# Performance work log

Hardware: AMD Instinct MI355X
Metric: run time of the kernel (lower is better)

The kernel has to match this reference:

```python
import jax, jax.numpy as jnp
import numpy as np

B = 8
S_MAX = 1024
H = 12
HD = 64
D = H * HD
DFF = 4 * D
NEG = -1.0e9  # matches Triton kernel's -1000000000.0 mask value


def _layernorm(x, g, b, eps=1e-6):
    mu = jnp.mean(x, axis=-1, keepdims=True)
    var = jnp.mean((x - mu) ** 2, axis=-1, keepdims=True)
    return (x - mu) * jax.lax.rsqrt(var + eps) * g + b


def setup_inputs() -> dict:
    key = jax.random.key(0)
    ks = jax.random.split(key, 12)
    lengths = np.array([1024, 896, 768, 640, 896, 1024, 512, 384], dtype=np.int32)
    assert lengths.max() <= S_MAX and len(lengths) == B
    total = int(lengths.sum())  # 6144
    cu = jnp.asarray(np.concatenate([[0], np.cumsum(lengths)]), dtype=jnp.int32)
    s = 0.02
    return {
        "x": jax.random.normal(ks[0], (total, D), jnp.float32),
        "cu_seqlens": cu,
        "g1": jnp.ones((D,), jnp.float32),
        "beta1": jnp.zeros((D,), jnp.float32),
        "Wqkv": jax.random.normal(ks[1], (D, 3 * D), jnp.float32) * s,
        "bqkv": jnp.zeros((3 * D,), jnp.float32),
        "Wo": jax.random.normal(ks[2], (D, D), jnp.float32) * s,
        "bo": jnp.zeros((D,), jnp.float32),
        "g2": jnp.ones((D,), jnp.float32),
        "beta2": jnp.zeros((D,), jnp.float32),
        "W1": jax.random.normal(ks[3], (D, DFF), jnp.float32) * s,
        "b_fc1": jnp.zeros((DFF,), jnp.float32),
        "W2": jax.random.normal(ks[4], (DFF, D), jnp.float32) * s,
        "b_fc2": jnp.zeros((D,), jnp.float32),
    }


def _ragged_attention(q, k, v, cu_seqlens):
    # q,k,v: [Total, H, HD] packed ragged sequences; cu_seqlens: [B+1] int32
    total = q.shape[0]
    lens = cu_seqlens[1:] - cu_seqlens[:-1]                      # [B]
    s = jnp.arange(S_MAX)
    pad_idx = cu_seqlens[:-1, None] + jnp.minimum(s[None, :], lens[:, None] - 1)  # [B,S]
    valid = s[None, :] < lens[:, None]                           # [B,S]
    qp = q[pad_idx]                                              # [B,S,H,HD]
    kp = k[pad_idx]
    vp = v[pad_idx]
    scale = 1.0 / jnp.sqrt(jnp.float32(HD))
    scores = jnp.einsum("bqhd,bkhd->bhqk", qp, kp) * scale      # [B,H,S,S]
    scores = jnp.where(valid[:, None, None, :], scores, NEG)     # mask invalid keys
    p = jax.nn.softmax(scores, axis=-1)
    op = jnp.einsum("bhqk,bkhd->bqhd", p, vp)                   # [B,S,H,HD]
    # repack to [Total, H, HD]
    tok = jnp.arange(total)
    seg = jnp.searchsorted(cu_seqlens, tok, side="right") - 1    # sequence id per token
    pos = tok - cu_seqlens[seg]
    return op[seg, pos]


def _forward(x, cu_seqlens, g1, beta1, Wqkv, bqkv, Wo, bo, g2, beta2, W1, b_fc1, W2, b_fc2):
    total = x.shape[0]
    qkv = (_layernorm(x, g1, beta1) @ Wqkv + bqkv).reshape(total, 3, H, HD)
    q, k, v = qkv[:, 0], qkv[:, 1], qkv[:, 2]
    attn = _ragged_attention(q, k, v, cu_seqlens).reshape(total, D)
    x = x + (attn @ Wo + bo)                                     # proj_drop/ls1/drop_path identity (eval)
    h = _layernorm(x, g2, beta2)
    m = jax.nn.gelu(h @ W1 + b_fc1, approximate=False)
    return x + (m @ W2 + b_fc2)


def reference(x, cu_seqlens, g1, beta1, Wqkv, bqkv, Wo, bo, g2, beta2, W1, b_fc1, W2, b_fc2):
    return _forward(x, cu_seqlens, g1, beta1, Wqkv, bqkv, Wo, bo, g2, beta2, W1, b_fc1, W2, b_fc2)
```

## Files before the change

kernel.cpp:

```cpp
#include <hip/hip_runtime.h>
#include <hip/hip_bf16.h>
#include <stdint.h>
#include <string.h>

#define D_MODEL 768
#define H_HEADS 12
#define HD_ 64
#define N_QKV 2304

typedef __bf16 bf16x8 __attribute__((ext_vector_type(8)));
typedef float f32x4 __attribute__((ext_vector_type(4)));

__device__ __forceinline__ unsigned short f2bfbits(float f) {
  union { float f; unsigned u; } x; x.f = f;
  unsigned r = x.u + 0x7fffu + ((x.u >> 16) & 1u);
  return (unsigned short)(r >> 16);
}

__device__ __forceinline__ unsigned pk2(float a, float b) {
  union { float f; unsigned u; } x, y; x.f = a; y.f = b;
  return ((x.u + 0x8000u) >> 16) | ((y.u + 0x8000u) & 0xffff0000u);
}

#define FENCE_() __builtin_amdgcn_sched_barrier(0)
__device__ __forceinline__ void store_sync() {
  FENCE_();
  asm volatile("s_waitcnt lgkmcnt(0)");
  FENCE_();
  __builtin_amdgcn_s_barrier();
  FENCE_();
}

__global__ void transpose_w(const float* __restrict__ in, unsigned short* __restrict__ out,
                            int R, int C) {
  __shared__ float tile[32][33];
  int c0 = blockIdx.x * 32, r0 = blockIdx.y * 32;
  int tx = threadIdx.x, ty = threadIdx.y;
#pragma unroll
  for (int i = 0; i < 32; i += 8)
    tile[ty + i][tx] = in[(size_t)(r0 + ty + i) * C + c0 + tx];
  __syncthreads();
#pragma unroll
  for (int i = 0; i < 32; i += 8)
    out[(size_t)(c0 + ty + i) * R + r0 + tx] = f2bfbits(tile[tx][ty + i]);
}

__global__ void transpose_v(const unsigned short* __restrict__ qkv,
                            unsigned short* __restrict__ vT, int M) {
  __shared__ unsigned short tile[32][33];
  int t0 = blockIdx.x * 32, c0 = blockIdx.y * 32;
  int tx = threadIdx.x, ty = threadIdx.y;
#pragma unroll
  for (int i = 0; i < 32; i += 8)
    tile[ty + i][tx] = qkv[(size_t)(t0 + ty + i) * N_QKV + 1536 + c0 + tx];
  __syncthreads();
  int t = t0 + tx;
  int c = t & 63;
  int kp = ((c >> 5) << 5) | (((c >> 2) & 3) << 3) | (((c >> 4) & 1) << 2) | (c & 3);
  size_t col = (size_t)(t & ~63) + kp;
#pragma unroll
  for (int i = 0; i < 32; i += 8)
    vT[(size_t)(c0 + ty + i) * M + col] = tile[tx][ty + i];
}

__global__ void ln_bf16(const float* __restrict__ x, const float* __restrict__ g,
                        const float* __restrict__ be, unsigned short* __restrict__ out) {
  int row = blockIdx.x;
  const float* xr = x + (size_t)row * D_MODEL;
  int t = threadIdx.x;
  float v0 = xr[t], v1 = xr[t + 256], v2 = xr[t + 512];
  float s = v0 + v1 + v2;
  float s2 = v0 * v0 + v1 * v1 + v2 * v2;
#pragma unroll
  for (int off = 32; off > 0; off >>= 1) {
    s += __shfl_down(s, off, 64);
    s2 += __shfl_down(s2, off, 64);
  }
  __shared__ float red[8];
  int w = t >> 6, lane = t & 63;
  if (lane == 0) { red[w] = s; red[w + 4] = s2; }
  __syncthreads();
  if (t == 0) {
    float a = red[0] + red[1] + red[2] + red[3];
    float b = red[4] + red[5] + red[6] + red[7];
    red[0] = a * (1.0f / 768.0f);
    red[4] = b * (1.0f / 768.0f);
  }
  __syncthreads();
  float mu = red[0];
  float var = red[4] - mu * mu;
  float rs = rsqrtf(var + 1e-6f);
  unsigned short* orow = out + (size_t)row * D_MODEL;
  orow[t]       = f2bfbits((v0 - mu) * rs * g[t]       + be[t]);
  orow[t + 256] = f2bfbits((v1 - mu) * rs * g[t + 256] + be[t + 256]);
  orow[t + 512] = f2bfbits((v2 - mu) * rs * g[t + 512] + be[t + 512]);
}

template <int EPI>
__global__ void __launch_bounds__(256, 3)
gemm_rs(const unsigned short* __restrict__ A,
        const unsigned short* __restrict__ Bt,
        const float* __restrict__ bias,
        const float* __restrict__ res,
        void* __restrict__ outv,
        int M, int N, int K) {
  __shared__ unsigned short lA[2][128 * 32];
  __shared__ unsigned short lB[2][128 * 32];
  int tid = threadIdx.x;
  int w = tid >> 6, lane = tid & 63;
  int id = blockIdx.x;
  int nn = N >> 7, bandM = (M >> 7) >> 3;
  int xcd = id & 7, s = id >> 3;
  int mt = xcd * bandM + s / nn;
  int nt = s - (s / nn) * nn;
  int m0 = mt * 128, n0 = nt * 128;
  int wm = (w >> 1) * 64, wn = (w & 1) * 64;
  f32x4 acc[4][4];
#pragma unroll
  for (int i = 0; i < 4; i++)
#pragma unroll
    for (int j = 0; j < 4; j++) acc[i][j] = (f32x4){0.f, 0.f, 0.f, 0.f};

  int sr = tid >> 2, sc = tid & 3;
  const unsigned short* gA = A + (size_t)(m0 + sr) * K + sc * 8;
  const unsigned short* gB = Bt + (size_t)(n0 + sr) * K + sc * 8;
  int wOff = sr * 64 + ((((sr >> 1) & 3) ^ sc) * 16);
  int fm = lane & 15, fg = lane >> 4;

  uint4 pA0, pA1, pB0, pB1;
  uint4 qA0, qA1, qB0, qB1;

  int nk = K >> 5;
  pA0 = *(const uint4*)(gA);
  pA1 = *(const uint4*)(gA + (size_t)64 * K);
  pB0 = *(const uint4*)(gB);
  pB1 = *(const uint4*)(gB + (size_t)64 * K);
  qA0 = *(const uint4*)(gA + 32);
  qA1 = *(const uint4*)(gA + (size_t)64 * K + 32);
  qB0 = *(const uint4*)(gB + 32);
  qB1 = *(const uint4*)(gB + (size_t)64 * K + 32);

  for (int k = 0; k < nk; k += 2) {
    {
      char* la = (char*)&lA[0][0];
      char* lb = (char*)&lB[0][0];
      *(uint4*)(la + wOff) = pA0;
      *(uint4*)(la + wOff + 4096) = pA1;
      *(uint4*)(lb + wOff) = pB0;
      *(uint4*)(lb + wOff + 4096) = pB1;
      if (k + 2 < nk) {
        int k0 = (k + 2) * 32;
        pA0 = *(const uint4*)(gA + k0);
        pA1 = *(const uint4*)(gA + (size_t)64 * K + k0);
        pB0 = *(const uint4*)(gB + k0);
        pB1 = *(const uint4*)(gB + (size_t)64 * K + k0);
      }
      store_sync();
      bf16x8 af[4], bfr[4];
#pragma unroll
      for (int i = 0; i < 4; i++) {
        int rr = wm + i * 16 + fm;
        af[i] = *(const bf16x8*)(la + rr * 64 + ((((rr >> 1) & 3) ^ fg) * 16));
      }
#pragma unroll
      for (int j = 0; j < 4; j++) {
        int rr = wn + j * 16 + fm;
        bfr[j] = *(const bf16x8*)(lb + rr * 64 + ((((rr >> 1) & 3) ^ fg) * 16));
      }
#pragma unroll
      for (int i = 0; i < 4; i++)
#pragma unroll
        for (int j = 0; j < 4; j++)
          acc[i][j] = __builtin_amdgcn_mfma_f32_16x16x32_bf16(af[i], bfr[j], acc[i][j], 0, 0, 0);
      store_sync();
    }
    {
      char* la = (char*)&lA[1][0];
      char* lb = (char*)&lB[1][0];
      *(uint4*)(la + wOff) = qA0;
      *(uint4*)(la + wOff + 4096) = qA1;
      *(uint4*)(lb + wOff) = qB0;
      *(uint4*)(lb + wOff + 4096) = qB1;
      if (k + 3 < nk) {
        int k0 = (k + 3) * 32;
        qA0 = *(const uint4*)(gA + k0);
        qA1 = *(const uint4*)(gA + (size_t)64 * K + k0);
        qB0 = *(const uint4*)(gB + k0);
        qB1 = *(const uint4*)(gB + (size_t)64 * K + k0);
      }
      store_sync();
      bf16x8 af[4], bfr[4];
#pragma unroll
      for (int i = 0; i < 4; i++) {
        int rr = wm + i * 16 + fm;
        af[i] = *(const bf16x8*)(la + rr * 64 + ((((rr >> 1) & 3) ^ fg) * 16));
      }
#pragma unroll
      for (int j = 0; j < 4; j++) {
        int rr = wn + j * 16 + fm;
        bfr[j] = *(const bf16x8*)(lb + rr * 64 + ((((rr >> 1) & 3) ^ fg) * 16));
      }
#pragma unroll
      for (int i = 0; i < 4; i++)
#pragma unroll
        for (int j = 0; j < 4; j++)
          acc[i][j] = __builtin_amdgcn_mfma_f32_16x16x32_bf16(af[i], bfr[j], acc[i][j], 0, 0, 0);
      store_sync();
    }
  }

  int er = (lane >> 4) * 4, ec = lane & 15;
#pragma unroll
  for (int i = 0; i < 4; i++) {
#pragma unroll
    for (int j = 0; j < 4; j++) {
      int n = n0 + wn + j * 16 + ec;
      float bv = bias[n];
#pragma unroll
      for (int r = 0; r < 4; r++) {
        int m = m0 + wm + i * 16 + er + r;
        float v = acc[i][j][r] + bv;
        if (EPI == 1) {
          v += res[(size_t)m * N + n];
          ((float*)outv)[(size_t)m * N + n] = v;
        } else {
          if (EPI == 2) v = 0.5f * v * (1.0f + erff(v * 0.70710678118f));
          ((unsigned short*)outv)[(size_t)m * N + n] = f2bfbits(v);
        }
      }
    }
  }
}

__global__ void attn_flash4(const unsigned short* __restrict__ qkv,
                            const unsigned short* __restrict__ vT,
                            const int* __restrict__ cu,
                            unsigned short* __restrict__ out, int M) {
  int id = blockIdx.x;
  int qc = id / 96;
  int bh = id - qc * 96;
  int b = bh / 12, h = bh - b * 12;
  int tok0 = cu[b];
  int len = cu[b + 1] - tok0;
  if (qc * 128 >= len) return;

  __shared__ unsigned short lK[2][64 * 64];
  __shared__ unsigned short lVT[2][64 * 64];

  int tid = threadIdx.x, w = tid >> 6, lane = tid & 63;
  int fm = lane & 15, fg = lane >> 4;
  int xm = fm & 7;
  int qbase = qc * 128 + w * 32;

  bf16x8 qf[2][2];
#pragma unroll
  for (int qs = 0; qs < 2; qs++)
#pragma unroll
    for (int kh = 0; kh < 2; kh++)
      qf[qs][kh] = *(const bf16x8*)(qkv + (size_t)(tok0 + qbase + qs * 16 + fm) * N_QKV +
                                    h * 64 + kh * 32 + fg * 8);

  f32x4 Oacc[2][4];
#pragma unroll
  for (int qs = 0; qs < 2; qs++)
#pragma unroll
    for (int dt = 0; dt < 4; dt++) Oacc[qs][dt] = (f32x4){0.f, 0.f, 0.f, 0.f};
  float lrow[2] = {0.f, 0.f};
  const float C2 = 0.18033688011112042f;

  int sr = tid >> 3, sp = tid & 7, sl = sp ^ (sr & 7);
  const unsigned short* kg0 = qkv + D_MODEL + h * 64 + sl * 8;
  const unsigned short* vg0 = vT + (size_t)(h * 64 + sr) * M + tok0 + sl * 8;

  uint4 rk0, rk1, rv0, rv1;
  auto gload = [&](int kt) {
    rk0 = *(const uint4*)(kg0 + (size_t)(tok0 + kt + sr) * N_QKV);
    rk1 = *(const uint4*)(kg0 + (size_t)(tok0 + kt + sr + 32) * N_QKV);
    rv0 = *(const uint4*)(vg0 + kt);
    rv1 = *(const uint4*)(vg0 + (size_t)32 * M + kt);
  };

  int nkt = len >> 6;
  gload(0);
  for (int kt = 0; kt < nkt; kt++) {
    int cur = kt & 1;
    *(uint4*)((char*)&lK[cur][0] + tid * 16) = rk0;
    *(uint4*)((char*)&lK[cur][0] + tid * 16 + 4096) = rk1;
    *(uint4*)((char*)&lVT[cur][0] + tid * 16) = rv0;
    *(uint4*)((char*)&lVT[cur][0] + tid * 16 + 4096) = rv1;
    if (kt + 1 < nkt) gload((kt + 1) * 64);
    store_sync();

    f32x4 s[2][4];
#pragma unroll
    for (int qs = 0; qs < 2; qs++)
#pragma unroll
      for (int t = 0; t < 4; t++) s[qs][t] = (f32x4){0.f, 0.f, 0.f, 0.f};
#pragma unroll
    for (int t = 0; t < 4; t++) {
      bf16x8 kf0 = *(const bf16x8*)&lK[cur][(t * 16 + fm) * 64 + ((fg ^ xm) * 8)];
      bf16x8 kf1 = *(const bf16x8*)&lK[cur][(t * 16 + fm) * 64 + (((4 + fg) ^ xm) * 8)];
#pragma unroll
      for (int qs = 0; qs < 2; qs++) {
        s[qs][t] = __builtin_amdgcn_mfma_f32_16x16x32_bf16(kf0, qf[qs][0], s[qs][t], 0, 0, 0);
        s[qs][t] = __builtin_amdgcn_mfma_f32_16x16x32_bf16(kf1, qf[qs][1], s[qs][t], 0, 0, 0);
      }
    }

    union { bf16x8 v; unsigned u[4]; } af[2][2];
#pragma unroll
    for (int qs = 0; qs < 2; qs++) {
      float ssum = 0.f;
#pragma unroll
      for (int t = 0; t < 4; t++) {
#pragma unroll
        for (int r = 0; r < 4; r++) {
          float p = exp2f(s[qs][t][r] * C2);
          s[qs][t][r] = p;
          ssum += p;
        }
      }
      lrow[qs] += ssum;
      af[qs][0].u[0] = pk2(s[qs][0][0], s[qs][0][1]);
      af[qs][0].u[1] = pk2(s[qs][0][2], s[qs][0][3]);
      af[qs][0].u[2] = pk2(s[qs][1][0], s[qs][1][1]);
      af[qs][0].u[3] = pk2(s[qs][1][2], s[qs][1][3]);
      af[qs][1].u[0] = pk2(s[qs][2][0], s[qs][2][1]);
      af[qs][1].u[1] = pk2(s[qs][2][2], s[qs][2][3]);
      af[qs][1].u[2] = pk2(s[qs][3][0], s[qs][3][1]);
      af[qs][1].u[3] = pk2(s[qs][3][2], s[qs][3][3]);
    }

#pragma unroll
    for (int dt = 0; dt < 4; dt++) {
      bf16x8 vf0 = *(const bf16x8*)&lVT[cur][(dt * 16 + fm) * 64 + ((fg ^ xm) * 8)];
      bf16x8 vf1 = *(const bf16x8*)&lVT[cur][(dt * 16 + fm) * 64 + (((4 + fg) ^ xm) * 8)];
#pragma unroll
      for (int qs = 0; qs < 2; qs++) {
        Oacc[qs][dt] = __builtin_amdgcn_mfma_f32_16x16x32_bf16(af[qs][0].v, vf0, Oacc[qs][dt], 0, 0, 0);
        Oacc[qs][dt] = __builtin_amdgcn_mfma_f32_16x16x32_bf16(af[qs][1].v, vf1, Oacc[qs][dt], 0, 0, 0);
      }
    }
  }

#pragma unroll
  for (int qs = 0; qs < 2; qs++) {
    lrow[qs] += __shfl_xor(lrow[qs], 16, 64);
    lrow[qs] += __shfl_xor(lrow[qs], 32, 64);
    float inv = 1.0f / lrow[qs];
    float ir[4];
#pragma unroll
    for (int r = 0; r < 4; r++) ir[r] = __shfl(inv, fg * 4 + r, 64);
#pragma unroll
    for (int dt = 0; dt < 4; dt++)
#pragma unroll
      for (int r = 0; r < 4; r++)
        out[(size_t)(tok0 + qbase + qs * 16 + fg * 4 + r) * D_MODEL + h * 64 + dt * 16 + fm] =
            f2bfbits(Oacc[qs][dt][r] * ir[r]);
  }
}

extern "C" void kernel_launch(void* const* d_in, const int* in_sizes, int n_in,
                              void* d_out, int out_size, void* d_ws, size_t ws_size,
                              hipStream_t stream) {
  const float* x    = (const float*)d_in[0];
  const int* cu     = (const int*)d_in[1];
  const float* g1   = (const float*)d_in[2];
  const float* be1  = (const float*)d_in[3];
  const float* Wqkv = (const float*)d_in[4];
  const float* bqkv = (const float*)d_in[5];
  const float* Wo   = (const float*)d_in[6];
  const float* bo   = (const float*)d_in[7];
  const float* g2   = (const float*)d_in[8];
  const float* be2  = (const float*)d_in[9];
  const float* W1   = (const float*)d_in[10];
  const float* bfc1 = (const float*)d_in[11];
  const float* W2   = (const float*)d_in[12];
  const float* bfc2 = (const float*)d_in[13];
  float* out = (float*)d_out;
  int M = in_sizes[0] / D_MODEL;

  unsigned short* WqkvT = (unsigned short*)d_ws;
  unsigned short* WoT   = WqkvT + 2304 * 768;
  unsigned short* W1T   = WoT + 768 * 768;
  unsigned short* W2T   = W1T + 3072 * 768;
  unsigned short* bufA  = W2T + 768 * 3072;
  float* x1             = (float*)(bufA + (size_t)M * D_MODEL);
  unsigned short* qkvb  = (unsigned short*)(x1 + (size_t)M * D_MODEL);
  unsigned short* vT = (unsigned short*)x1;

  dim3 b32(32, 8);
  transpose_w<<<dim3(2304 / 32, 768 / 32), b32, 0, stream>>>(Wqkv, WqkvT, 768, 2304);
  transpose_w<<<dim3(768 / 32, 768 / 32), b32, 0, stream>>>(Wo, WoT, 768, 768);
  transpose_w<<<dim3(3072 / 32, 768 / 32), b32, 0, stream>>>(W1, W1T, 768, 3072);
  transpose_w<<<dim3(768 / 32, 3072 / 32), b32, 0, stream>>>(W2, W2T, 3072, 768);

  ln_bf16<<<M, 256, 0, stream>>>(x, g1, be1, bufA);
  gemm_rs<0><<<(2304 / 128) * (M / 128), 256, 0, stream>>>(bufA, WqkvT, bqkv, nullptr, qkvb, M, 2304, 768);
  transpose_v<<<dim3(M / 32, 768 / 32), b32, 0, stream>>>(qkvb, vT, M);
  attn_flash4<<<8 * 96, 256, 0, stream>>>(qkvb, vT, cu, bufA, M);
  gemm_rs<1><<<(768 / 128) * (M / 128), 256, 0, stream>>>(bufA, WoT, bo, x, x1, M, 768, 768);
  ln_bf16<<<M, 256, 0, stream>>>(x1, g2, be2, bufA);
  gemm_rs<2><<<(3072 / 128) * (M / 128), 256, 0, stream>>>(bufA, W1T, bfc1, nullptr, qkvb, M, 3072, 768);
  gemm_rs<1><<<(768 / 128) * (M / 128), 256, 0, stream>>>(qkvb, W2T, bfc2, x1, out, M, 768, 3072);
}
```

Before: 344.7 us.

## Use direct global-to-LDS loads in GEMM and add 128x64 tile kernel

The GEMM main loop now issues global_load_lds so tiles go straight from global memory into shared memory. It double-buffers them with vmcnt-based waits, which removes the register staging and explicit LDS stores. A new gemm_n64 variant with a 128x64 tile is used for the two N=768 projections (Wo and FC2). That doubles the block count so more CUs are busy on those narrow GEMMs. The tradeoff is tighter manual synchronisation, and the swizzle is applied on the global read side, which must stay consistent with the fragment reads.

```diff
diff --git a/kernel.cpp b/kernel.cpp
--- a/kernel.cpp
+++ b/kernel.cpp
@@ -10,6 +10,7 @@
 
 typedef __bf16 bf16x8 __attribute__((ext_vector_type(8)));
 typedef float f32x4 __attribute__((ext_vector_type(4)));
+typedef __attribute__((address_space(3))) char lds_char;
 
 __device__ __forceinline__ unsigned short f2bfbits(float f) {
   union { float f; unsigned u; } x; x.f = f;
@@ -21,6 +22,15 @@
   union { float f; unsigned u; } x, y; x.f = a; y.f = b;
   return ((x.u + 0x8000u) >> 16) | ((y.u + 0x8000u) & 0xffff0000u);
 }
+
+__device__ __forceinline__ void gload_lds16(const void* g, void* l) {
+  __builtin_amdgcn_global_load_lds(
+      (const __attribute__((address_space(1))) unsigned int*)g,
+      (__attribute__((address_space(3))) unsigned int*)l, 16, 0, 0);
+}
+
+#define DSR(dst, ptr, IMM) \
+  asm volatile("ds_read_b128 %0, %1 offset:%2" : "=v"(dst) : "v"(ptr), "n"(IMM))
 
 #define FENCE_() __builtin_amdgcn_sched_barrier(0)
 __device__ __forceinline__ void store_sync() {
@@ -121,93 +131,57 @@
 #pragma unroll
     for (int j = 0; j < 4; j++) acc[i][j] = (f32x4){0.f, 0.f, 0.f, 0.f};
 
-  int sr = tid >> 2, sc = tid & 3;
-  const unsigned short* gA = A + (size_t)(m0 + sr) * K + sc * 8;
-  const unsigned short* gB = Bt + (size_t)(n0 + sr) * K + sc * 8;
-  int wOff = sr * 64 + ((((sr >> 1) & 3) ^ sc) * 16);
   int fm = lane & 15, fg = lane >> 4;
 
-  uint4 pA0, pA1, pB0, pB1;
-  uint4 qA0, qA1, qB0, qB1;
-
+  int r0s = w * 16 + (lane >> 2);
+  int sc0 = (lane & 3) ^ ((r0s >> 1) & 3);
+  const unsigned short* gAs = A + (size_t)(m0 + r0s) * K + sc0 * 8;
+  const unsigned short* gBs = Bt + (size_t)(n0 + r0s) * K + sc0 * 8;
+  char* lA0 = (char*)&lA[0][0];
+  char* lB0 = (char*)&lB[0][0];
+  int wo = w * 1024;
   int nk = K >> 5;
-  pA0 = *(const uint4*)(gA);
-  pA1 = *(const uint4*)(gA + (size_t)64 * K);
-  pB0 = *(const uint4*)(gB);
-  pB1 = *(const uint4*)(gB + (size_t)64 * K);
-  qA0 = *(const uint4*)(gA + 32);
-  qA1 = *(const uint4*)(gA + (size_t)64 * K + 32);
-  qB0 = *(const uint4*)(gB + 32);
-  qB1 = *(const uint4*)(gB + (size_t)64 * K + 32);
-
-  for (int k = 0; k < nk; k += 2) {
-    {
-      char* la = (char*)&lA[0][0];
-      char* lb = (char*)&lB[0][0];
-      *(uint4*)(la + wOff) = pA0;
-      *(uint4*)(la + wOff + 4096) = pA1;
-      *(uint4*)(lb + wOff) = pB0;
-      *(uint4*)(lb + wOff + 4096) = pB1;
-      if (k + 2 < nk) {
-        int k0 = (k + 2) * 32;
-        pA0 = *(const uint4*)(gA + k0);
-        pA1 = *(const uint4*)(gA + (size_t)64 * K + k0);
-        pB0 = *(const uint4*)(gB + k0);
-        pB1 = *(const uint4*)(gB + (size_t)64 * K + k0);
-      }
-      store_sync();
-      bf16x8 af[4], bfr[4];
-#pragma unroll
-      for (int i = 0; i < 4; i++) {
-        int rr = wm + i * 16 + fm;
-        af[i] = *(const bf16x8*)(la + rr * 64 + ((((rr >> 1) & 3) ^ fg) * 16));
-      }
-#pragma unroll
-      for (int j = 0; j < 4; j++) {
-        int rr = wn + j * 16 + fm;
-        bfr[j] = *(const bf16x8*)(lb + rr * 64 + ((((rr >> 1) & 3) ^ fg) * 16));
-      }
-#pragma unroll
-      for (int i = 0; i < 4; i++)
-#pragma unroll
-        for (int j = 0; j < 4; j++)
-          acc[i][j] = __builtin_amdgcn_mfma_f32_16x16x32_bf16(af[i], bfr[j], acc[i][j], 0, 0, 0);
-      store_sync();
-    }
-    {
-      char* la = (char*)&lA[1][0];
-      char* lb = (char*)&lB[1][0];
-      *(uint4*)(la + wOff) = qA0;
-      *(uint4*)(la + wOff + 4096) = qA1;
-      *(uint4*)(lb + wOff) = qB0;
-      *(uint4*)(lb + wOff + 4096) = qB1;
-      if (k + 3 < nk) {
-        int k0 = (k + 3) * 32;
-        qA0 = *(const uint4*)(gA + k0);
-        qA1 = *(const uint4*)(gA + (size_t)64 * K + k0);
-        qB0 = *(const uint4*)(gB + k0);
-        qB1 = *(const uint4*)(gB + (size_t)64 * K + k0);
-      }
-      store_sync();
-      bf16x8 af[4], bfr[4];
-#pragma unroll
-      for (int i = 0; i < 4; i++) {
-        int rr = wm + i * 16 + fm;
-        af[i] = *(const bf16x8*)(la + rr * 64 + ((((rr >> 1) & 3) ^ fg) * 16));
-      }
-#pragma unroll
-      for (int j = 0; j < 4; j++) {
-        int rr = wn + j * 16 + fm;
-        bfr[j] = *(const bf16x8*)(lb + rr * 64 + ((((rr >> 1) & 3) ^ fg) * 16));
-      }
-#pragma unroll
-      for (int i = 0; i < 4; i++)
-#pragma unroll
-        for (int j = 0; j < 4; j++)
-          acc[i][j] = __builtin_amdgcn_mfma_f32_16x16x32_bf16(af[i], bfr[j], acc[i][j], 0, 0, 0);
-      store_sync();
-    }
-  }
+
+  auto stage = [&](int kt, int buf) {
+    int kk = kt < nk ? kt : nk - 1;
+    int off = kk * 32;
+    gload_lds16(gAs + off,                  lA0 + buf * 8192 + wo);
+    gload_lds16(gAs + off + (size_t)64 * K, lA0 + buf * 8192 + 4096 + wo);
+    gload_lds16(gBs + off,                  lB0 + buf * 8192 + wo);
+    gload_lds16(gBs + off + (size_t)64 * K, lB0 + buf * 8192 + 4096 + wo);
+  };
+
+  const unsigned aoff0 = (unsigned)((wm + fm) * 64 + ((((wm + fm) >> 1) & 3) ^ fg) * 16);
+  const unsigned boff0 = (unsigned)((wn + fm) * 64 + ((((wn + fm) >> 1) & 3) ^ fg) * 16);
+
+  stage(0, 0);
+  stage(1, 1);
+
+  for (int k = 0; k < nk; ++k) {
+    int cur = k & 1;
+    asm volatile("s_waitcnt vmcnt(4)");
+    FENCE_();
+    __builtin_amdgcn_s_barrier();
+    FENCE_();
+    bf16x8 af[4], bfr[4];
+    const lds_char* pa = (const lds_char*)(lA0 + cur * 8192 + aoff0);
+    const lds_char* pb = (const lds_char*)(lB0 + cur * 8192 + boff0);
+    DSR(af[0], pa, 0); DSR(af[1], pa, 1024); DSR(af[2], pa, 2048); DSR(af[3], pa, 3072);
+    DSR(bfr[0], pb, 0); DSR(bfr[1], pb, 1024); DSR(bfr[2], pb, 2048); DSR(bfr[3], pb, 3072);
+    asm volatile("s_waitcnt lgkmcnt(0)");
+    FENCE_();
+    __builtin_amdgcn_s_barrier();
+    FENCE_();
+    stage(k + 2, cur);
+    FENCE_();
+#pragma unroll
+    for (int i = 0; i < 4; ++i)
+#pragma unroll
+      for (int j = 0; j < 4; ++j)
+        acc[i][j] = __builtin_amdgcn_mfma_f32_16x16x32_bf16(af[i], bfr[j], acc[i][j], 0, 0, 0);
+  }
+  asm volatile("s_waitcnt vmcnt(0)");
+  FENCE_();
 
   int er = (lane >> 4) * 4, ec = lane & 15;
 #pragma unroll
@@ -215,6 +189,105 @@
 #pragma unroll
     for (int j = 0; j < 4; j++) {
       int n = n0 + wn + j * 16 + ec;
+      float bv = bias[n];
+#pragma unroll
+      for (int r = 0; r < 4; r++) {
+        int m = m0 + wm + i * 16 + er + r;
+        float v = acc[i][j][r] + bv;
+        if (EPI == 1) {
+          v += res[(size_t)m * N + n];
+          ((float*)outv)[(size_t)m * N + n] = v;
+        } else {
+          if (EPI == 2) v = 0.5f * v * (1.0f + erff(v * 0.70710678118f));
+          ((unsigned short*)outv)[(size_t)m * N + n] = f2bfbits(v);
+        }
+      }
+    }
+  }
+}
+
+template <int EPI>
+__global__ void __launch_bounds__(256, 4)
+gemm_n64(const unsigned short* __restrict__ A,
+         const unsigned short* __restrict__ Bt,
+         const float* __restrict__ bias,
+         const float* __restrict__ res,
+         void* __restrict__ outv,
+         int M, int N, int K) {
+  __shared__ unsigned short lA[2][128 * 32];
+  __shared__ unsigned short lB[2][64 * 32];
+  int tid = threadIdx.x;
+  int w = tid >> 6, lane = tid & 63;
+  int id = blockIdx.x;
+  int nn = N >> 6, bandM = (M >> 7) >> 3;
+  int xcd = id & 7, s = id >> 3;
+  int mt = xcd * bandM + s / nn;
+  int nt = s - (s / nn) * nn;
+  int m0 = mt * 128, n0 = nt * 64;
+  int wm = w * 32;
+  f32x4 acc[2][4];
+#pragma unroll
+  for (int i = 0; i < 2; i++)
+#pragma unroll
+    for (int j = 0; j < 4; j++) acc[i][j] = (f32x4){0.f, 0.f, 0.f, 0.f};
+
+  int fm = lane & 15, fg = lane >> 4;
+
+  int r0s = w * 16 + (lane >> 2);
+  int sc0 = (lane & 3) ^ ((r0s >> 1) & 3);
+  const unsigned short* gAs = A + (size_t)(m0 + r0s) * K + sc0 * 8;
+  const unsigned short* gBs = Bt + (size_t)(n0 + r0s) * K + sc0 * 8;
+  char* lA0 = (char*)&lA[0][0];
+  char* lB0 = (char*)&lB[0][0];
+  int wo = w * 1024;
+  int nk = K >> 5;
+
+  auto stage = [&](int kt, int buf) {
+    int kk = kt < nk ? kt : nk - 1;
+    int off = kk * 32;
+    gload_lds16(gAs + off,                  lA0 + buf * 8192 + wo);
+    gload_lds16(gAs + off + (size_t)64 * K, lA0 + buf * 8192 + 4096 + wo);
+    gload_lds16(gBs + off,                  lB0 + buf * 4096 + wo);
+  };
+
+  const unsigned aoff0 = (unsigned)((wm + fm) * 64 + ((((wm + fm) >> 1) & 3) ^ fg) * 16);
+  const unsigned boff0 = (unsigned)(fm * 64 + (((fm >> 1) & 3) ^ fg) * 16);
+
+  stage(0, 0);
+  stage(1, 1);
+
+  for (int k = 0; k < nk; ++k) {
+    int cur = k & 1;
+    asm volatile("s_waitcnt vmcnt(3)");
+    FENCE_();
+    __builtin_amdgcn_s_barrier();
+    FENCE_();
+    bf16x8 af[2], bfr[4];
+    const lds_char* pa = (const lds_char*)(lA0 + cur * 8192 + aoff0);
+    const lds_char* pb = (const lds_char*)(lB0 + cur * 4096 + boff0);
+    DSR(af[0], pa, 0); DSR(af[1], pa, 1024);
+    DSR(bfr[0], pb, 0); DSR(bfr[1], pb, 1024); DSR(bfr[2], pb, 2048); DSR(bfr[3], pb, 3072);
+    asm volatile("s_waitcnt lgkmcnt(0)");
+    FENCE_();
+    __builtin_amdgcn_s_barrier();
+    FENCE_();
+    stage(k + 2, cur);
+    FENCE_();
+#pragma unroll
+    for (int i = 0; i < 2; ++i)
+#pragma unroll
+      for (int j = 0; j < 4; ++j)
+        acc[i][j] = __builtin_amdgcn_mfma_f32_16x16x32_bf16(af[i], bfr[j], acc[i][j], 0, 0, 0);
+  }
+  asm volatile("s_waitcnt vmcnt(0)");
+  FENCE_();
+
+  int er = (lane >> 4) * 4, ec = lane & 15;
+#pragma unroll
+  for (int i = 0; i < 2; i++) {
+#pragma unroll
+    for (int j = 0; j < 4; j++) {
+      int n = n0 + j * 16 + ec;
       float bv = bias[n];
 #pragma unroll
       for (int r = 0; r < 4; r++) {
@@ -399,8 +472,8 @@
   gemm_rs<0><<<(2304 / 128) * (M / 128), 256, 0, stream>>>(bufA, WqkvT, bqkv, nullptr, qkvb, M, 2304, 768);
   transpose_v<<<dim3(M / 32, 768 / 32), b32, 0, stream>>>(qkvb, vT, M);
   attn_flash4<<<8 * 96, 256, 0, stream>>>(qkvb, vT, cu, bufA, M);
-  gemm_rs<1><<<(768 / 128) * (M / 128), 256, 0, stream>>>(bufA, WoT, bo, x, x1, M, 768, 768);
+  gemm_n64<1><<<(768 / 64) * (M / 128), 256, 0, stream>>>(bufA, WoT, bo, x, x1, M, 768, 768);
   ln_bf16<<<M, 256, 0, stream>>>(x1, g2, be2, bufA);
   gemm_rs<2><<<(3072 / 128) * (M / 128), 256, 0, stream>>>(bufA, W1T, bfc1, nullptr, qkvb, M, 3072, 768);
-  gemm_rs<1><<<(768 / 128) * (M / 128), 256, 0, stream>>>(qkvb, W2T, bfc2, x1, out, M, 768, 3072);
-}
+  gemm_n64<1><<<(768 / 64) * (M / 128), 256, 0, stream>>>(qkvb, W2T, bfc2, x1, out, M, 768, 3072);
+}
```

Result: no change. 351.4 us (+1.9%).
